# Kernel tuning notes

Measured on AMD Instinct MI355X. Metric: run time of the kernel, lower is better.

Reference implementation:

```python
import jax, jax.numpy as jnp
import numpy as np

B = 16
PATCH_NUM = 32      # L of inter branch
PATCH_SIZE = 128    # L of intra branch
WIN_SIZE = PATCH_NUM * PATCH_SIZE  # 4096
H = 8
E = 64


def setup_inputs() -> dict:
    key = jax.random.key(0)
    ks = jax.random.split(key, 6)
    return {
        "q_inter": jax.random.normal(ks[0], (B, PATCH_NUM, H, E), jnp.float32),
        "k_inter": jax.random.normal(ks[1], (B, PATCH_NUM, H, E), jnp.float32),
        "v_inter": jax.random.normal(ks[2], (B, PATCH_NUM, H, E), jnp.float32),
        "q_intra": jax.random.normal(ks[3], (B, PATCH_SIZE, H, E), jnp.float32),
        "k_intra": jax.random.normal(ks[4], (B, PATCH_SIZE, H, E), jnp.float32),
        "v_intra": jax.random.normal(ks[5], (B, PATCH_SIZE, H, E), jnp.float32),
    }


def _full_attention(q, k, v):
    # q,k,v: [B, L, H, E]; full softmax attention, scale = 1/sqrt(E)
    scale = 1.0 / jnp.sqrt(jnp.asarray(q.shape[-1], q.dtype))
    score = jnp.einsum('blhe,bshe->bhls', q, k) * scale
    att = jax.nn.softmax(score, axis=-1)  # dropout is identity in eval mode
    return jnp.einsum('bhls,bshd->blhd', att, v)


def reference(q_inter, k_inter, v_inter, q_intra, k_intra, v_intra):
    V_inter = _full_attention(q_inter, k_inter, v_inter)  # [B, patch_num, H, E]
    V_intra = _full_attention(q_intra, k_intra, v_intra)  # [B, patch_size, H, E]
    # einops repeat 'b pn h d -> b (pn ps) h d': each patch repeated ps times
    V_inter_up = jnp.repeat(V_inter, PATCH_SIZE, axis=1)  # [B, win_size, H, E]
    # einops repeat 'b ps h d -> b (ps pn) h d': each position repeated pn times
    V_intra_up = jnp.repeat(V_intra, PATCH_NUM, axis=1)   # [B, win_size, H, E]
    return V_inter_up + V_intra_up
```

## Files before the change

### kernel.cpp

```cpp
#include <hip/hip_runtime.h>


#define NH 8
#define NE 64
#define ROWSTRIDE (NH * NE)

typedef float vf4 __attribute__((ext_vector_type(4)));

__device__ __forceinline__ float dot4(const float4 a, const float4 b) {
    return a.x * b.x + a.y * b.y + a.z * b.z + a.w * b.w;
}

__global__ __launch_bounds__(256, 2) void temp_attn_mega(
    const float* __restrict__ qI, const float* __restrict__ kI, const float* __restrict__ vI,
    const float* __restrict__ qT, const float* __restrict__ kT, const float* __restrict__ vT,
    float* __restrict__ out)
{
    __shared__ __align__(16) float sKs[128 * 68];
    __shared__ __align__(16) float sVs[128 * 64];
    __shared__ __align__(16) float sQs[32 * 68];
    __shared__ __align__(16) float sIO[8 * 68];

    const int tid  = threadIdx.x;
    const int bid  = blockIdx.x;
    const int tile = bid & 3;
    const int h    = (bid >> 2) & 7;
    const int b    = bid >> 5;
    const int r0   = tile * 32;
    const int pn0  = tile * 8;

    {
        const float* kg = kI + ((size_t)b * 32 * NH + h) * NE;
        const float* vg = vI + ((size_t)b * 32 * NH + h) * NE;
        float* dK = sKs;
        float* dV = sKs + 32 * 68;
        for (int idx = tid; idx < 32 * 16; idx += 256) {
            const int row = idx >> 4;
            const int f   = (idx & 15) * 4;
            *(float4*)&dK[row * 68 + f] = *(const float4*)(kg + (size_t)row * ROWSTRIDE + f);
            *(float4*)&dV[row * 64 + f] = *(const float4*)(vg + (size_t)row * ROWSTRIDE + f);
        }
    }
    __syncthreads();
    {
        const int rg = tid >> 5;
        const int ln = tid & 31;
        const float* dK = sKs;
        const float* dV = sKs + 32 * 68;

        const float* qrow = qI + ((size_t)(b * 32 + pn0 + rg) * NH + h) * NE;
        float s = 0.f;
        #pragma unroll
        for (int e = 0; e < NE; e += 4) {
            const float4 qv = *(const float4*)(qrow + e);
            const float4 kv = *(const float4*)&dK[ln * 68 + e];
            s += dot4(qv, kv);
        }
        s *= 0.125f;
        float m = s;
        #pragma unroll
        for (int msk = 1; msk < 32; msk <<= 1) m = fmaxf(m, __shfl_xor(m, msk));
        const float p = __expf(s - m);
        float sum = p;
        #pragma unroll
        for (int msk = 1; msk < 32; msk <<= 1) sum += __shfl_xor(sum, msk);
        const float pn = p / sum;

        const int hw = tid & 32;
        float o0 = 0.f, o1 = 0.f;
        #pragma unroll 8
        for (int c = 0; c < 32; c++) {
            const float pc = __shfl(pn, hw + c);
            const float2 v = *(const float2*)&dV[c * 64 + ln * 2];
            o0 += pc * v.x;
            o1 += pc * v.y;
        }
        sIO[rg * 68 + ln * 2]     = o0;
        sIO[rg * 68 + ln * 2 + 1] = o1;
    }
    __syncthreads();

    {
        const float* kg = kT + ((size_t)b * 128 * NH + h) * NE;
        const float* vg = vT + ((size_t)b * 128 * NH + h) * NE;
        const float* qg = qT + ((size_t)(b * 128 + r0) * NH + h) * NE;
        for (int idx = tid; idx < 128 * 16; idx += 256) {
            const int row = idx >> 4;
            const int f   = (idx & 15) * 4;
            *(float4*)&sKs[row * 68 + f] = *(const float4*)(kg + (size_t)row * ROWSTRIDE + f);
            *(float4*)&sVs[row * 64 + f] = *(const float4*)(vg + (size_t)row * ROWSTRIDE + f);
        }
        for (int idx = tid; idx < 32 * 16; idx += 256) {
            const int row = idx >> 4;
            const int f   = (idx & 15) * 4;
            *(float4*)&sQs[row * 68 + f] = *(const float4*)(qg + (size_t)row * ROWSTRIDE + f);
        }
    }
    __syncthreads();

    const int rg = tid >> 5;
    const int cg = tid & 31;
    const int rr = rg * 4;
    float acc[4][4];
    #pragma unroll
    for (int i = 0; i < 4; i++)
        #pragma unroll
        for (int j = 0; j < 4; j++) acc[i][j] = 0.f;

    #pragma unroll
    for (int e = 0; e < NE; e += 4) {
        float4 qv[4], kv[4];
        #pragma unroll
        for (int i = 0; i < 4; i++) qv[i] = *(const float4*)&sQs[(rr + i) * 68 + e];
        #pragma unroll
        for (int j = 0; j < 4; j++) kv[j] = *(const float4*)&sKs[(cg + j * 32) * 68 + e];
        #pragma unroll
        for (int i = 0; i < 4; i++)
            #pragma unroll
            for (int j = 0; j < 4; j++)
                acc[i][j] += dot4(qv[i], kv[j]);
    }
    __syncthreads();

    float* S = sKs;

    #pragma unroll
    for (int i = 0; i < 4; i++) {
        float m = acc[i][0] * 0.125f;
        #pragma unroll
        for (int j = 1; j < 4; j++) m = fmaxf(m, acc[i][j] * 0.125f);
        #pragma unroll
        for (int msk = 1; msk < 32; msk <<= 1) m = fmaxf(m, __shfl_xor(m, msk));
        float p[4], s = 0.f;
        #pragma unroll
        for (int j = 0; j < 4; j++) { p[j] = __expf(acc[i][j] * 0.125f - m); s += p[j]; }
        #pragma unroll
        for (int msk = 1; msk < 32; msk <<= 1) s += __shfl_xor(s, msk);
        const float inv = 1.f / s;
        #pragma unroll
        for (int j = 0; j < 4; j++)
            S[(rr + i) * 132 + cg + 32 * j] = p[j] * inv;
    }
    __syncthreads();

    const int r   = tid >> 3;
    const int sub = tid & 7;
    const int e0  = sub * 8;
    float a0=0,a1=0,a2=0,a3=0,a4=0,a5=0,a6=0,a7=0;
    for (int c0 = 0; c0 < 128; c0 += 4) {
        const float4 p4 = *(const float4*)&S[r * 132 + c0];
        const float pv[4] = { p4.x, p4.y, p4.z, p4.w };
        #pragma unroll
        for (int u = 0; u < 4; u++) {
            const float p  = pv[u];
            const float4 va = *(const float4*)&sVs[(c0 + u) * 64 + e0];
            const float4 vb = *(const float4*)&sVs[(c0 + u) * 64 + e0 + 4];
            a0 += p * va.x; a1 += p * va.y; a2 += p * va.z; a3 += p * va.w;
            a4 += p * vb.x; a5 += p * vb.y; a6 += p * vb.z; a7 += p * vb.w;
        }
    }

    const int io = (r >> 2) * 68 + e0;
    const float4 iA = *(const float4*)&sIO[io];
    const float4 iB = *(const float4*)&sIO[io + 4];
    vf4 oA, oB;
    oA.x = a0 + iA.x; oA.y = a1 + iA.y; oA.z = a2 + iA.z; oA.w = a3 + iA.w;
    oB.x = a4 + iB.x; oB.y = a5 + iB.y; oB.z = a6 + iB.z; oB.w = a7 + iB.w;

    const int i = r0 + r;
    float* ob = out + ((size_t)(b * 4096 + i * 32) * NH + h) * NE + e0;
    #pragma unroll
    for (int j = 0; j < 32; j++) {
        __builtin_nontemporal_store(oA, (vf4*)(ob + (size_t)j * ROWSTRIDE));
        __builtin_nontemporal_store(oB, (vf4*)(ob + (size_t)j * ROWSTRIDE + 4));
    }
}

extern "C" void kernel_launch(void* const* d_in, const int* in_sizes, int n_in,
                              void* d_out, int out_size, void* d_ws, size_t ws_size,
                              hipStream_t stream) {
    const float* q_inter = (const float*)d_in[0];
    const float* k_inter = (const float*)d_in[1];
    const float* v_inter = (const float*)d_in[2];
    const float* q_intra = (const float*)d_in[3];
    const float* k_intra = (const float*)d_in[4];
    const float* v_intra = (const float*)d_in[5];
    float* out = (float*)d_out;
    (void)d_ws; (void)ws_size;

    temp_attn_mega<<<512, 256, 0, stream>>>(
        q_inter, k_inter, v_inter, q_intra, k_intra, v_intra, out);
}
```

Baseline: 205.2 us.

## Split attention from output broadcast and compute PV via readlane broadcasts

The single fused kernel becomes two. The first computes the combined inter and intra attention rows into a compact workspace: it prefetches intra V and Q alongside the inter loads, drops the shared-memory probability matrix and one barrier, and forms P·V by broadcasting probabilities from registers with readlane. A second kernel reads the workspace and writes each row 32 times to the output with nontemporal stores. The aim is to separate the compute phase from the store-bound broadcast so the broadcast runs across more blocks with simple streaming writes. The cost is an extra launch, a workspace round trip, and losing the overlap of compute with output writes that the fused kernel had.

```diff
diff --git a/kernel.cpp b/kernel.cpp
--- a/kernel.cpp
+++ b/kernel.cpp
@@ -11,10 +11,14 @@
     return a.x * b.x + a.y * b.y + a.z * b.z + a.w * b.w;
 }
 
-__global__ __launch_bounds__(256, 2) void temp_attn_mega(
+__device__ __forceinline__ float readlane_f(float v, int lane) {
+    return __uint_as_float(__builtin_amdgcn_readlane(__float_as_uint(v), lane));
+}
+
+__global__ __launch_bounds__(256, 2) void attn_combined(
     const float* __restrict__ qI, const float* __restrict__ kI, const float* __restrict__ vI,
     const float* __restrict__ qT, const float* __restrict__ kT, const float* __restrict__ vT,
-    float* __restrict__ out)
+    float* __restrict__ wsSum)
 {
     __shared__ __align__(16) float sKs[128 * 68];
     __shared__ __align__(16) float sVs[128 * 64];
@@ -40,8 +44,21 @@
             *(float4*)&dK[row * 68 + f] = *(const float4*)(kg + (size_t)row * ROWSTRIDE + f);
             *(float4*)&dV[row * 64 + f] = *(const float4*)(vg + (size_t)row * ROWSTRIDE + f);
         }
+        const float* vgT = vT + ((size_t)b * 128 * NH + h) * NE;
+        for (int idx = tid; idx < 128 * 16; idx += 256) {
+            const int row = idx >> 4;
+            const int f   = (idx & 15) * 4;
+            *(float4*)&sVs[row * 64 + f] = *(const float4*)(vgT + (size_t)row * ROWSTRIDE + f);
+        }
+        const float* qgT = qT + ((size_t)(b * 128 + r0) * NH + h) * NE;
+        for (int idx = tid; idx < 32 * 16; idx += 256) {
+            const int row = idx >> 4;
+            const int f   = (idx & 15) * 4;
+            *(float4*)&sQs[row * 68 + f] = *(const float4*)(qgT + (size_t)row * ROWSTRIDE + f);
+        }
     }
     __syncthreads();
+
     {
         const int rg = tid >> 5;
         const int ln = tid & 31;
@@ -60,11 +77,11 @@
         float m = s;
         #pragma unroll
         for (int msk = 1; msk < 32; msk <<= 1) m = fmaxf(m, __shfl_xor(m, msk));
-        const float p = __expf(s - m);
-        float sum = p;
+        const float pe = __expf(s - m);
+        float sum = pe;
         #pragma unroll
         for (int msk = 1; msk < 32; msk <<= 1) sum += __shfl_xor(sum, msk);
-        const float pn = p / sum;
+        const float pn = pe / sum;
 
         const int hw = tid & 32;
         float o0 = 0.f, o1 = 0.f;
@@ -81,19 +98,11 @@
     __syncthreads();
 
     {
-        const float* kg = kT + ((size_t)b * 128 * NH + h) * NE;
-        const float* vg = vT + ((size_t)b * 128 * NH + h) * NE;
-        const float* qg = qT + ((size_t)(b * 128 + r0) * NH + h) * NE;
+        const float* kgT = kT + ((size_t)b * 128 * NH + h) * NE;
         for (int idx = tid; idx < 128 * 16; idx += 256) {
             const int row = idx >> 4;
             const int f   = (idx & 15) * 4;
-            *(float4*)&sKs[row * 68 + f] = *(const float4*)(kg + (size_t)row * ROWSTRIDE + f);
-            *(float4*)&sVs[row * 64 + f] = *(const float4*)(vg + (size_t)row * ROWSTRIDE + f);
-        }
-        for (int idx = tid; idx < 32 * 16; idx += 256) {
-            const int row = idx >> 4;
-            const int f   = (idx & 15) * 4;
-            *(float4*)&sQs[row * 68 + f] = *(const float4*)(qg + (size_t)row * ROWSTRIDE + f);
+            *(float4*)&sKs[row * 68 + f] = *(const float4*)(kgT + (size_t)row * ROWSTRIDE + f);
         }
     }
     __syncthreads();
@@ -120,10 +129,8 @@
             for (int j = 0; j < 4; j++)
                 acc[i][j] += dot4(qv[i], kv[j]);
     }
-    __syncthreads();
-
-    float* S = sKs;
-
+
+    float p[4][4];
     #pragma unroll
     for (int i = 0; i < 4; i++) {
         float m = acc[i][0] * 0.125f;
@@ -131,49 +138,56 @@
         for (int j = 1; j < 4; j++) m = fmaxf(m, acc[i][j] * 0.125f);
         #pragma unroll
         for (int msk = 1; msk < 32; msk <<= 1) m = fmaxf(m, __shfl_xor(m, msk));
-        float p[4], s = 0.f;
-        #pragma unroll
-        for (int j = 0; j < 4; j++) { p[j] = __expf(acc[i][j] * 0.125f - m); s += p[j]; }
+        float s = 0.f;
+        #pragma unroll
+        for (int j = 0; j < 4; j++) { p[i][j] = __expf(acc[i][j] * 0.125f - m); s += p[i][j]; }
         #pragma unroll
         for (int msk = 1; msk < 32; msk <<= 1) s += __shfl_xor(s, msk);
         const float inv = 1.f / s;
         #pragma unroll
-        for (int j = 0; j < 4; j++)
-            S[(rr + i) * 132 + cg + 32 * j] = p[j] * inv;
-    }
-    __syncthreads();
-
-    const int r   = tid >> 3;
-    const int sub = tid & 7;
-    const int e0  = sub * 8;
-    float a0=0,a1=0,a2=0,a3=0,a4=0,a5=0,a6=0,a7=0;
-    for (int c0 = 0; c0 < 128; c0 += 4) {
-        const float4 p4 = *(const float4*)&S[r * 132 + c0];
-        const float pv[4] = { p4.x, p4.y, p4.z, p4.w };
-        #pragma unroll
-        for (int u = 0; u < 4; u++) {
-            const float p  = pv[u];
-            const float4 va = *(const float4*)&sVs[(c0 + u) * 64 + e0];
-            const float4 vb = *(const float4*)&sVs[(c0 + u) * 64 + e0 + 4];
-            a0 += p * va.x; a1 += p * va.y; a2 += p * va.z; a3 += p * va.w;
-            a4 += p * vb.x; a5 += p * vb.y; a6 += p * vb.z; a7 += p * vb.w;
-        }
-    }
-
-    const int io = (r >> 2) * 68 + e0;
-    const float4 iA = *(const float4*)&sIO[io];
-    const float4 iB = *(const float4*)&sIO[io + 4];
-    vf4 oA, oB;
-    oA.x = a0 + iA.x; oA.y = a1 + iA.y; oA.z = a2 + iA.z; oA.w = a3 + iA.w;
-    oB.x = a4 + iB.x; oB.y = a5 + iB.y; oB.z = a6 + iB.z; oB.w = a7 + iB.w;
-
-    const int i = r0 + r;
-    float* ob = out + ((size_t)(b * 4096 + i * 32) * NH + h) * NE + e0;
-    #pragma unroll
-    for (int j = 0; j < 32; j++) {
-        __builtin_nontemporal_store(oA, (vf4*)(ob + (size_t)j * ROWSTRIDE));
-        __builtin_nontemporal_store(oB, (vf4*)(ob + (size_t)j * ROWSTRIDE + 4));
-    }
+        for (int j = 0; j < 4; j++) p[i][j] *= inv;
+    }
+
+    const int lane = tid & 63;
+    const int w    = tid >> 6;
+    float accE[8] = {0.f, 0.f, 0.f, 0.f, 0.f, 0.f, 0.f, 0.f};
+
+    for (int j = 0; j < 4; j++) {
+        #pragma unroll
+        for (int cc = 0; cc < 32; cc++) {
+            const float v = sVs[(j * 32 + cc) * 64 + lane];
+            #pragma unroll
+            for (int i = 0; i < 8; i++) {
+                const float pc = readlane_f(p[i & 3][j], (i >> 2) * 32 + cc);
+                accE[i] = fmaf(pc, v, accE[i]);
+            }
+        }
+    }
+
+    #pragma unroll
+    for (int i = 0; i < 8; i++) {
+        const float vin = sIO[(2 * w + (i >> 2)) * 68 + lane];
+        const int   row = r0 + 8 * w + i;
+        wsSum[((size_t)(b * 128 + row) * NH + h) * NE + lane] = accE[i] + vin;
+    }
+}
+
+__global__ __launch_bounds__(256) void duplicate_kernel(
+    const float4* __restrict__ ws, float* __restrict__ out)
+{
+    const int t  = blockIdx.x * 256 + threadIdx.x;
+    const int e4 = t & 15;
+    const int h  = (t >> 4) & 7;
+    const int pi = (t >> 7) & 127;
+    const int b  = t >> 14;
+
+    const float4 a = ws[((b * 128 + pi) * NH + h) * 16 + e4];
+    vf4 s; s.x = a.x; s.y = a.y; s.z = a.z; s.w = a.w;
+
+    float* o = out + ((((size_t)b * 4096 + pi * 32) * NH + h) * 16 + e4) * 4;
+    #pragma unroll
+    for (int j = 0; j < 32; j++)
+        __builtin_nontemporal_store(s, (vf4*)(o + (size_t)j * ROWSTRIDE));
 }
 
 extern "C" void kernel_launch(void* const* d_in, const int* in_sizes, int n_in,
@@ -186,8 +200,10 @@
     const float* k_intra = (const float*)d_in[4];
     const float* v_intra = (const float*)d_in[5];
     float* out = (float*)d_out;
-    (void)d_ws; (void)ws_size;
-
-    temp_attn_mega<<<512, 256, 0, stream>>>(
-        q_inter, k_inter, v_inter, q_intra, k_intra, v_intra, out);
-}
+    float* ws  = (float*)d_ws;
+
+    attn_combined<<<512, 256, 0, stream>>>(
+        q_inter, k_inter, v_inter, q_intra, k_intra, v_intra, ws);
+
+    duplicate_kernel<<<1024, 256, 0, stream>>>((const float4*)ws, out);
+}
```

Result: faster. 178.0 us (-13.2%).
